# Performance work log

Hardware: AMD Instinct MI355X
Metric: run time of the kernel (lower is better)

## Reference

```python
import jax, jax.numpy as jnp
import numpy as np

HEADS = 16
HEAD_DIM = 64  # hidden_dim // heads = 1024 // 16


def setup_inputs() -> dict:
    key = jax.random.key(0)
    ks = jax.random.split(key, 7)
    B, S, D = 2, 2048, 1024
    x = jax.random.normal(ks[0], (B, S, D), dtype=jnp.float32)
    mask = jax.random.randint(ks[1], (B, 1, S, S), 0, 2, dtype=jnp.int32)
    scale = 1.0 / np.sqrt(D)
    Wq = jax.random.normal(ks[2], (D, D), dtype=jnp.float32) * scale
    Wk = jax.random.normal(ks[3], (D, D), dtype=jnp.float32) * scale
    Wv = jax.random.normal(ks[4], (D, D), dtype=jnp.float32) * scale
    Wo = jax.random.normal(ks[5], (D, D), dtype=jnp.float32) * scale
    bo = jnp.zeros((D,), dtype=jnp.float32)
    return {"x": x, "mask": mask, "Wq": Wq, "Wk": Wk, "Wv": Wv, "Wo": Wo, "bo": bo}


def _split_heads(t):
    # (B, S, D) -> (B, H, S, Hd)
    B, S, D = t.shape
    return t.reshape(B, S, HEADS, HEAD_DIM).transpose(0, 2, 1, 3)


def reference(x, mask, Wq, Wk, Wv, Wo, bo):
    B, S, D = x.shape
    # torch nn.Linear: y = x @ W.T (weights stored [out, in])
    q = _split_heads(x @ Wq.T)
    k = _split_heads(x @ Wk.T)
    v = _split_heads(x @ Wv.T)
    scores = jnp.einsum("bhqd,bhkd->bhqk", q, k) / jnp.sqrt(jnp.float32(HEAD_DIM))
    scores = jnp.where(mask == 1, jnp.float32(-1e9), scores)
    attn = jax.nn.softmax(scores, axis=-1)
    # dropout p=0.0 (eval) -> identity
    out = jnp.einsum("bhqk,bhkd->bhqd", attn, v)
    out = out.transpose(0, 2, 1, 3).reshape(B, S, D)
    return out @ Wo.T + bo
```

## Files before the change

kernel.cpp:

```cpp
#include <hip/hip_runtime.h>
#include <hip/hip_bf16.h>

typedef __attribute__((ext_vector_type(4))) float f32x4;
typedef __attribute__((ext_vector_type(8))) short bf16x8;

#define MFMA16(a, b, c) __builtin_amdgcn_mfma_f32_16x16x32_bf16(a, b, c, 0, 0, 0)

#define AS1(p) ((const __attribute__((address_space(1))) void*)(p))
#define AS3(p) ((__attribute__((address_space(3))) void*)(p))

#define SWZ(r) ((((r) & 7)) ^ ((((r) >> 3) & 1) << 2))

__device__ __forceinline__ unsigned short f2bf(float f) {
  union { float f; unsigned u; } x; x.f = f;
  unsigned r = x.u + 0x7fffu + ((x.u >> 16) & 1u);
  return (unsigned short)(r >> 16);
}

__global__ __launch_bounds__(256) void convert_all(
    const float* __restrict__ x, const float* __restrict__ wq,
    const float* __restrict__ wk, const float* __restrict__ wv,
    const float* __restrict__ wo, unsigned short* __restrict__ dst) {
  const int NX = 4194304, NW = 1048576, TOT = NX + 4 * NW;
  for (int i = blockIdx.x * 256 + threadIdx.x; i < TOT; i += gridDim.x * 256) {
    float v;
    if (i < NX) {
      v = x[i];
    } else {
      int j = i - NX; int ws = j >> 20; int o = j & (NW - 1);
      v = (ws == 0) ? wq[o] : (ws == 1) ? wk[o] : (ws == 2) ? wv[o] : wo[o];
    }
    dst[i] = f2bf(v);
  }
}

__global__ __launch_bounds__(256) void convert_mask(
    const int* __restrict__ m, unsigned char* __restrict__ o) {
  const int i = blockIdx.x * 256 + threadIdx.x;
  const int4 v = ((const int4*)m)[i];
  uchar4 r;
  r.x = (unsigned char)v.x; r.y = (unsigned char)v.y;
  r.z = (unsigned char)v.z; r.w = (unsigned char)v.w;
  ((uchar4*)o)[i] = r;
}

__device__ __forceinline__ void gemm_nt_128(
    const unsigned short* __restrict__ A, const unsigned short* __restrict__ Bw,
    int m0, int n0, unsigned short* Al, unsigned short* Bl, f32x4 acc[4][4]) {
  const int t = threadIdx.x;
  const int l = t & 63;
  const int w = t >> 6, wr = w >> 1, wc = w & 1;
  const int lc = l & 15, lg = l >> 4;

  auto stage = [&](int buf, int kt) {
    const int k0 = kt * 32;
#pragma unroll
    for (int c = 0; c < 2; ++c) {
      const int e = (t + c * 256) * 8;
      const int row = e >> 5, col = e & 31;
      __builtin_amdgcn_global_load_lds(
          AS1(A + (size_t)(m0 + row) * 1024 + k0 + col),
          AS3(Al + buf * 4096 + (w * 64 + c * 256) * 8), 16, 0, 0);
      __builtin_amdgcn_global_load_lds(
          AS1(Bw + (size_t)(n0 + row) * 1024 + k0 + col),
          AS3(Bl + buf * 4096 + (w * 64 + c * 256) * 8), 16, 0, 0);
    }
  };

  stage(0, 0);
#pragma unroll 2
  for (int kt = 0; kt < 32; ++kt) {
    __syncthreads();
    if (kt + 1 < 32) stage((kt + 1) & 1, kt + 1);
    const unsigned short* Ab = Al + (kt & 1) * 4096;
    const unsigned short* Bb = Bl + (kt & 1) * 4096;
    bf16x8 af[4], bfr[4];
#pragma unroll
    for (int i = 0; i < 4; ++i)
      af[i] = *(const bf16x8*)(Ab + (wr * 64 + i * 16 + lc) * 32 + lg * 8);
#pragma unroll
    for (int j = 0; j < 4; ++j)
      bfr[j] = *(const bf16x8*)(Bb + (wc * 64 + j * 16 + lc) * 32 + lg * 8);
#pragma unroll
    for (int i = 0; i < 4; ++i)
#pragma unroll
      for (int j = 0; j < 4; ++j)
        acc[i][j] = MFMA16(af[i], bfr[j], acc[i][j]);
  }
}

__global__ __launch_bounds__(256) void gemm_qkv(
    const unsigned short* __restrict__ xb,
    const unsigned short* __restrict__ wqb, const unsigned short* __restrict__ wkb,
    const unsigned short* __restrict__ wvb,
    unsigned short* __restrict__ q, unsigned short* __restrict__ k,
    unsigned short* __restrict__ vt) {
  __shared__ unsigned short Al[2 * 4096], Bl[2 * 4096];
  const int z = blockIdx.z;
  const unsigned short* Bw = (z == 0) ? wqb : (z == 1) ? wkb : wvb;
  const int m0 = blockIdx.x * 128, n0 = blockIdx.y * 128;
  f32x4 acc[4][4] = {};
  gemm_nt_128(xb, Bw, m0, n0, Al, Bl, acc);

  const int l = threadIdx.x & 63, w = threadIdx.x >> 6;
  const int wr = w >> 1, wc = w & 1, lc = l & 15, lg = l >> 4;

  if (z == 2) {
#pragma unroll
    for (int i = 0; i < 4; ++i)
#pragma unroll
      for (int j = 0; j < 4; ++j) {
        const int m = m0 + wr * 64 + i * 16 + lg * 4;
        const int n = n0 + wc * 64 + j * 16 + lc;
        const int b = m >> 11, s = m & 2047, hh = n >> 6, hd = n & 63;
        ushort4 pk;
        pk.x = f2bf(acc[i][j][0]); pk.y = f2bf(acc[i][j][1]);
        pk.z = f2bf(acc[i][j][2]); pk.w = f2bf(acc[i][j][3]);
        *(ushort4*)(vt + (size_t)((b << 4) + hh) * 131072 + (size_t)hd * 2048 + s) = pk;
      }
  } else {
    unsigned short* C = (z == 0) ? q : k;
#pragma unroll
    for (int i = 0; i < 4; ++i)
#pragma unroll
      for (int j = 0; j < 4; ++j)
#pragma unroll
        for (int r = 0; r < 4; ++r) {
          const int m = m0 + wr * 64 + i * 16 + lg * 4 + r;
          const int n = n0 + wc * 64 + j * 16 + lc;
          const int b = m >> 11, s = m & 2047, hh = n >> 6, hd = n & 63;
          C[(size_t)((b << 4) + hh) * 131072 + s * 64 + hd] = f2bf(acc[i][j][r]);
        }
  }
}

__global__ __launch_bounds__(256) void gemm_out(
    const unsigned short* __restrict__ ao, const unsigned short* __restrict__ wob,
    const float* __restrict__ bias, float* __restrict__ out) {
  __shared__ unsigned short Al[2 * 4096], Bl[2 * 4096];
  const int m0 = blockIdx.x * 128, n0 = blockIdx.y * 128;
  f32x4 acc[4][4] = {};
  gemm_nt_128(ao, wob, m0, n0, Al, Bl, acc);

  const int l = threadIdx.x & 63, w = threadIdx.x >> 6;
  const int wr = w >> 1, wc = w & 1, lc = l & 15, lg = l >> 4;
#pragma unroll
  for (int i = 0; i < 4; ++i)
#pragma unroll
    for (int j = 0; j < 4; ++j)
#pragma unroll
      for (int r = 0; r < 4; ++r) {
        const int m = m0 + wr * 64 + i * 16 + lg * 4 + r;
        const int n = n0 + wc * 64 + j * 16 + lc;
        out[(size_t)m * 1024 + n] = acc[i][j][r] + bias[n];
      }
}

__global__ __launch_bounds__(256, 4) void attn_fwd(
    const unsigned short* __restrict__ q, const unsigned short* __restrict__ k,
    const unsigned short* __restrict__ vt, const unsigned char* __restrict__ mb8,
    unsigned short* __restrict__ ao) {
  __shared__ unsigned short Kl[2][4096];
  __shared__ unsigned short Vl[2][4096];
  __shared__ unsigned short Pl[4][1024];
  const int orig = blockIdx.x;
  const int nid = (orig & 7) * 128 + (orig >> 3);
  const int bh = nid >> 5, b = bh >> 4;
  const int q0 = (nid & 31) * 64;
  const int t = threadIdx.x, l = t & 63, w = t >> 6;
  const int lc = l & 15, lg = l >> 4;

  const unsigned short* qp = q + ((size_t)bh * 2048 + q0 + w * 16) * 64;
  bf16x8 qa[2];
  qa[0] = *(const bf16x8*)(qp + lc * 64 + lg * 8);
  qa[1] = *(const bf16x8*)(qp + lc * 64 + 32 + lg * 8);

  bf16x8 onesf;
#pragma unroll
  for (int j = 0; j < 8; ++j) ((unsigned short*)&onesf)[j] = (lc == 0) ? 0x3F80 : 0;

  const unsigned short* kp = k + (size_t)bh * 131072;
  const unsigned short* vp = vt + (size_t)bh * 131072;
  const unsigned char* mp = mb8 + (size_t)b * 4194304 + (size_t)(q0 + w * 16 + lc) * 2048;

  f32x4 oa[4] = {};
  f32x4 lsum = {};

  auto stage = [&](int buf, int kv0) {
#pragma unroll
    for (int c = 0; c < 2; ++c) {
      const int ldc = (c * 4 + w) * 64 + l;
      const int row = ldc >> 3, ch = ldc & 7;
      const int sch = ch ^ SWZ(row);
      __builtin_amdgcn_global_load_lds(
          AS1(kp + (size_t)(kv0 + row) * 64 + sch * 8),
          AS3(&Kl[buf][(c * 4 + w) * 512]), 16, 0, 0);
      __builtin_amdgcn_global_load_lds(
          AS1(vp + (size_t)row * 2048 + kv0 + sch * 8),
          AS3(&Vl[buf][(c * 4 + w) * 512]), 16, 0, 0);
    }
  };

  stage(0, 0);
  for (int tt = 0; tt < 32; ++tt) {
    const int kv0 = tt * 64;
    __syncthreads();
    if (tt + 1 < 32) stage((tt + 1) & 1, kv0 + 64);
    const unsigned short* Kb = Kl[tt & 1];
    const unsigned short* Vb = Vl[tt & 1];

    f32x4 sa[4];
#pragma unroll
    for (int cb = 0; cb < 4; ++cb) {
      const unsigned mw = *(const unsigned*)(mp + kv0 + cb * 16 + lg * 4);
      sa[cb][0] = -240000.f * (float)(mw & 255u);
      sa[cb][1] = -240000.f * (float)((mw >> 8) & 255u);
      sa[cb][2] = -240000.f * (float)((mw >> 16) & 255u);
      sa[cb][3] = -240000.f * (float)(mw >> 24);
    }

#pragma unroll
    for (int cb = 0; cb < 4; ++cb) {
      const int row = cb * 16 + lc;
#pragma unroll
      for (int h2 = 0; h2 < 2; ++h2) {
        bf16x8 kf = *(const bf16x8*)(Kb + row * 64 + ((h2 * 4 + lg) ^ SWZ(row)) * 8);
        sa[cb] = MFMA16(kf, qa[h2], sa[cb]);
      }
    }

    unsigned short* Pw = (unsigned short*)Pl[w];
#pragma unroll
    for (int cb = 0; cb < 4; ++cb) {
      float2 ab, cd;
      ab.x = __builtin_amdgcn_exp2f(sa[cb][0] * 0.18033688f);
      ab.y = __builtin_amdgcn_exp2f(sa[cb][1] * 0.18033688f);
      cd.x = __builtin_amdgcn_exp2f(sa[cb][2] * 0.18033688f);
      cd.y = __builtin_amdgcn_exp2f(sa[cb][3] * 0.18033688f);
      __hip_bfloat162 lo = __float22bfloat162_rn(ab);
      __hip_bfloat162 hi = __float22bfloat162_rn(cd);
      uint2 pk;
      pk.x = *(unsigned*)&lo;
      pk.y = *(unsigned*)&hi;
      *(uint2*)(Pw + lc * 64 + ((cb * 2 + (lg >> 1)) ^ SWZ(lc)) * 8 + (lg & 1) * 4) = pk;
    }

#pragma unroll
    for (int kk = 0; kk < 2; ++kk) {
      bf16x8 pa = *(const bf16x8*)(Pw + lc * 64 + ((kk * 4 + lg) ^ SWZ(lc)) * 8);
      lsum = MFMA16(pa, onesf, lsum);
#pragma unroll
      for (int db = 0; db < 4; ++db) {
        const int d = db * 16 + lc;
        bf16x8 vf = *(const bf16x8*)(Vb + d * 64 + ((kk * 4 + lg) ^ SWZ(d)) * 8);
        oa[db] = MFMA16(pa, vf, oa[db]);
      }
    }
  }

  float li[4];
#pragma unroll
  for (int r = 0; r < 4; ++r) li[r] = __shfl(lsum[r], l & 48, 64);
#pragma unroll
  for (int r = 0; r < 4; ++r) {
    const float inv = 1.0f / li[r];
    const int row = q0 + w * 16 + lg * 4 + r;
    unsigned short* dst = ao + ((size_t)b * 2048 + row) * 1024 + (bh & 15) * 64;
#pragma unroll
    for (int db = 0; db < 4; ++db) dst[db * 16 + lc] = f2bf(oa[db][r] * inv);
  }
}

extern "C" void kernel_launch(void* const* d_in, const int* in_sizes, int n_in,
                              void* d_out, int out_size, void* d_ws, size_t ws_size,
                              hipStream_t stream) {
  const float* x = (const float*)d_in[0];
  const int* mask = (const int*)d_in[1];
  const float* Wq = (const float*)d_in[2];
  const float* Wk = (const float*)d_in[3];
  const float* Wv = (const float*)d_in[4];
  const float* Wo = (const float*)d_in[5];
  const float* bo = (const float*)d_in[6];

  unsigned short* ws = (unsigned short*)d_ws;
  unsigned short* xb = ws;
  unsigned short* wqb = xb + 4194304;
  unsigned short* wkb = wqb + 1048576;
  unsigned short* wvb = wkb + 1048576;
  unsigned short* wob = wvb + 1048576;
  unsigned short* qb = wob + 1048576;
  unsigned short* kb = qb + 4194304;
  unsigned short* vtb = kb + 4194304;
  unsigned short* aob = vtb + 4194304;

  unsigned char* mb8 = (unsigned char*)xb;

  convert_all<<<dim3(4096), dim3(256), 0, stream>>>(x, Wq, Wk, Wv, Wo, ws);
  gemm_qkv<<<dim3(32, 8, 3), dim3(256), 0, stream>>>(xb, wqb, wkb, wvb, qb, kb, vtb);
  convert_mask<<<dim3(8192), dim3(256), 0, stream>>>(mask, mb8);
  attn_fwd<<<dim3(1024), dim3(256), 0, stream>>>(qb, kb, vtb, mb8, aob);
  gemm_out<<<dim3(32, 8), dim3(256), 0, stream>>>(aob, wob, bo, (float*)d_out);
}
```

Measured before the change: 269.0 us.

## Vectorize conversion, shrink attention KV tile, use smaller out-proj tiles

The fp32-to-bf16 conversion kernel now has each thread convert 8 contiguous elements with float4 loads and one 16-byte store, replacing the grid-stride scalar loop. The attention kernel halves its K/V tile from 64 to 32 keys per iteration, adds a V-specific LDS swizzle, and raises the occupancy hint to 8 blocks per CU to improve latency hiding. The GEMM helper is templated so the output projection can use 64x128 tiles with twice as many blocks, which fills more CUs. The trade-off is more loop iterations and barriers in attention, and less data reuse per block in the output GEMM.

```diff
diff --git a/kernel.cpp b/kernel.cpp
--- a/kernel.cpp
+++ b/kernel.cpp
@@ -9,7 +9,8 @@
 #define AS1(p) ((const __attribute__((address_space(1))) void*)(p))
 #define AS3(p) ((__attribute__((address_space(3))) void*)(p))
 
-#define SWZ(r) ((((r) & 7)) ^ ((((r) >> 3) & 1) << 2))
+#define SWZK(r) ((((r) & 7)) ^ ((((r) >> 3) & 1) << 2))
+#define SWZV(r) ((((r) & 3)) ^ ((((r) >> 2) & 1) << 1))
 
 __device__ __forceinline__ unsigned short f2bf(float f) {
   union { float f; unsigned u; } x; x.f = f;
@@ -21,17 +22,23 @@
     const float* __restrict__ x, const float* __restrict__ wq,
     const float* __restrict__ wk, const float* __restrict__ wv,
     const float* __restrict__ wo, unsigned short* __restrict__ dst) {
-  const int NX = 4194304, NW = 1048576, TOT = NX + 4 * NW;
-  for (int i = blockIdx.x * 256 + threadIdx.x; i < TOT; i += gridDim.x * 256) {
-    float v;
-    if (i < NX) {
-      v = x[i];
-    } else {
-      int j = i - NX; int ws = j >> 20; int o = j & (NW - 1);
-      v = (ws == 0) ? wq[o] : (ws == 1) ? wk[o] : (ws == 2) ? wv[o] : wo[o];
-    }
-    dst[i] = f2bf(v);
-  }
+  const int i = blockIdx.x * 256 + threadIdx.x;
+  const long base = (long)i * 8;
+  const int NX = 4194304, NW = 1048576;
+  const float* src; long off;
+  if (base < NX) { src = x; off = base; }
+  else {
+    long j = base - NX; int ws = (int)(j >> 20); off = j & (NW - 1);
+    src = (ws == 0) ? wq : (ws == 1) ? wk : (ws == 2) ? wv : wo;
+  }
+  float4 a = *(const float4*)(src + off);
+  float4 b = *(const float4*)(src + off + 4);
+  uint4 o;
+  o.x = (unsigned)f2bf(a.x) | ((unsigned)f2bf(a.y) << 16);
+  o.y = (unsigned)f2bf(a.z) | ((unsigned)f2bf(a.w) << 16);
+  o.z = (unsigned)f2bf(b.x) | ((unsigned)f2bf(b.y) << 16);
+  o.w = (unsigned)f2bf(b.z) | ((unsigned)f2bf(b.w) << 16);
+  ((uint4*)dst)[i] = o;
 }
 
 __global__ __launch_bounds__(256) void convert_mask(
@@ -44,26 +51,32 @@
   ((uchar4*)o)[i] = r;
 }
 
-__device__ __forceinline__ void gemm_nt_128(
+template <int BM, int BN>
+__device__ __forceinline__ void gemm_nt(
     const unsigned short* __restrict__ A, const unsigned short* __restrict__ Bw,
-    int m0, int n0, unsigned short* Al, unsigned short* Bl, f32x4 acc[4][4]) {
+    int m0, int n0, unsigned short* Al, unsigned short* Bl, f32x4* acc) {
   const int t = threadIdx.x;
   const int l = t & 63;
   const int w = t >> 6, wr = w >> 1, wc = w & 1;
   const int lc = l & 15, lg = l >> 4;
+  constexpr int MI = BM / 32, NJ = BN / 32;
+  constexpr int ASZ = BM * 32, BSZ = BN * 32;
 
   auto stage = [&](int buf, int kt) {
     const int k0 = kt * 32;
 #pragma unroll
-    for (int c = 0; c < 2; ++c) {
+    for (int c = 0; c < BM / 64; ++c) {
       const int e = (t + c * 256) * 8;
-      const int row = e >> 5, col = e & 31;
       __builtin_amdgcn_global_load_lds(
-          AS1(A + (size_t)(m0 + row) * 1024 + k0 + col),
-          AS3(Al + buf * 4096 + (w * 64 + c * 256) * 8), 16, 0, 0);
+          AS1(A + (size_t)(m0 + (e >> 5)) * 1024 + k0 + (e & 31)),
+          AS3(Al + buf * ASZ + e), 16, 0, 0);
+    }
+#pragma unroll
+    for (int c = 0; c < BN / 64; ++c) {
+      const int e = (t + c * 256) * 8;
       __builtin_amdgcn_global_load_lds(
-          AS1(Bw + (size_t)(n0 + row) * 1024 + k0 + col),
-          AS3(Bl + buf * 4096 + (w * 64 + c * 256) * 8), 16, 0, 0);
+          AS1(Bw + (size_t)(n0 + (e >> 5)) * 1024 + k0 + (e & 31)),
+          AS3(Bl + buf * BSZ + e), 16, 0, 0);
     }
   };
 
@@ -72,20 +85,20 @@
   for (int kt = 0; kt < 32; ++kt) {
     __syncthreads();
     if (kt + 1 < 32) stage((kt + 1) & 1, kt + 1);
-    const unsigned short* Ab = Al + (kt & 1) * 4096;
-    const unsigned short* Bb = Bl + (kt & 1) * 4096;
-    bf16x8 af[4], bfr[4];
-#pragma unroll
-    for (int i = 0; i < 4; ++i)
-      af[i] = *(const bf16x8*)(Ab + (wr * 64 + i * 16 + lc) * 32 + lg * 8);
-#pragma unroll
-    for (int j = 0; j < 4; ++j)
-      bfr[j] = *(const bf16x8*)(Bb + (wc * 64 + j * 16 + lc) * 32 + lg * 8);
-#pragma unroll
-    for (int i = 0; i < 4; ++i)
-#pragma unroll
-      for (int j = 0; j < 4; ++j)
-        acc[i][j] = MFMA16(af[i], bfr[j], acc[i][j]);
+    const unsigned short* Ab = Al + (kt & 1) * ASZ;
+    const unsigned short* Bb = Bl + (kt & 1) * BSZ;
+    bf16x8 af[MI], bfr[NJ];
+#pragma unroll
+    for (int i = 0; i < MI; ++i)
+      af[i] = *(const bf16x8*)(Ab + (wr * (BM / 2) + i * 16 + lc) * 32 + lg * 8);
+#pragma unroll
+    for (int j = 0; j < NJ; ++j)
+      bfr[j] = *(const bf16x8*)(Bb + (wc * (BN / 2) + j * 16 + lc) * 32 + lg * 8);
+#pragma unroll
+    for (int i = 0; i < MI; ++i)
+#pragma unroll
+      for (int j = 0; j < NJ; ++j)
+        acc[i * NJ + j] = MFMA16(af[i], bfr[j], acc[i * NJ + j]);
   }
 }
 
@@ -99,8 +112,8 @@
   const int z = blockIdx.z;
   const unsigned short* Bw = (z == 0) ? wqb : (z == 1) ? wkb : wvb;
   const int m0 = blockIdx.x * 128, n0 = blockIdx.y * 128;
-  f32x4 acc[4][4] = {};
-  gemm_nt_128(xb, Bw, m0, n0, Al, Bl, acc);
+  f32x4 acc[16] = {};
+  gemm_nt<128, 128>(xb, Bw, m0, n0, Al, Bl, acc);
 
   const int l = threadIdx.x & 63, w = threadIdx.x >> 6;
   const int wr = w >> 1, wc = w & 1, lc = l & 15, lg = l >> 4;
@@ -114,8 +127,8 @@
         const int n = n0 + wc * 64 + j * 16 + lc;
         const int b = m >> 11, s = m & 2047, hh = n >> 6, hd = n & 63;
         ushort4 pk;
-        pk.x = f2bf(acc[i][j][0]); pk.y = f2bf(acc[i][j][1]);
-        pk.z = f2bf(acc[i][j][2]); pk.w = f2bf(acc[i][j][3]);
+        pk.x = f2bf(acc[i * 4 + j][0]); pk.y = f2bf(acc[i * 4 + j][1]);
+        pk.z = f2bf(acc[i * 4 + j][2]); pk.w = f2bf(acc[i * 4 + j][3]);
         *(ushort4*)(vt + (size_t)((b << 4) + hh) * 131072 + (size_t)hd * 2048 + s) = pk;
       }
   } else {
@@ -129,7 +142,7 @@
           const int m = m0 + wr * 64 + i * 16 + lg * 4 + r;
           const int n = n0 + wc * 64 + j * 16 + lc;
           const int b = m >> 11, s = m & 2047, hh = n >> 6, hd = n & 63;
-          C[(size_t)((b << 4) + hh) * 131072 + s * 64 + hd] = f2bf(acc[i][j][r]);
+          C[(size_t)((b << 4) + hh) * 131072 + s * 64 + hd] = f2bf(acc[i * 4 + j][r]);
         }
   }
 }
@@ -137,32 +150,32 @@
 __global__ __launch_bounds__(256) void gemm_out(
     const unsigned short* __restrict__ ao, const unsigned short* __restrict__ wob,
     const float* __restrict__ bias, float* __restrict__ out) {
-  __shared__ unsigned short Al[2 * 4096], Bl[2 * 4096];
-  const int m0 = blockIdx.x * 128, n0 = blockIdx.y * 128;
-  f32x4 acc[4][4] = {};
-  gemm_nt_128(ao, wob, m0, n0, Al, Bl, acc);
+  __shared__ unsigned short Al[2 * 2048], Bl[2 * 4096];
+  const int m0 = blockIdx.x * 64, n0 = blockIdx.y * 128;
+  f32x4 acc[8] = {};
+  gemm_nt<64, 128>(ao, wob, m0, n0, Al, Bl, acc);
 
   const int l = threadIdx.x & 63, w = threadIdx.x >> 6;
   const int wr = w >> 1, wc = w & 1, lc = l & 15, lg = l >> 4;
 #pragma unroll
-  for (int i = 0; i < 4; ++i)
+  for (int i = 0; i < 2; ++i)
 #pragma unroll
     for (int j = 0; j < 4; ++j)
 #pragma unroll
       for (int r = 0; r < 4; ++r) {
-        const int m = m0 + wr * 64 + i * 16 + lg * 4 + r;
+        const int m = m0 + wr * 32 + i * 16 + lg * 4 + r;
         const int n = n0 + wc * 64 + j * 16 + lc;
-        out[(size_t)m * 1024 + n] = acc[i][j][r] + bias[n];
+        out[(size_t)m * 1024 + n] = acc[i * 4 + j][r] + bias[n];
       }
 }
 
-__global__ __launch_bounds__(256, 4) void attn_fwd(
+__global__ __launch_bounds__(256, 8) void attn_fwd(
     const unsigned short* __restrict__ q, const unsigned short* __restrict__ k,
     const unsigned short* __restrict__ vt, const unsigned char* __restrict__ mb8,
     unsigned short* __restrict__ ao) {
-  __shared__ unsigned short Kl[2][4096];
-  __shared__ unsigned short Vl[2][4096];
-  __shared__ unsigned short Pl[4][1024];
+  __shared__ unsigned short Kl[2][2048];
+  __shared__ unsigned short Vl[2][2048];
+  __shared__ unsigned short Pl[4][512];
   const int orig = blockIdx.x;
   const int nid = (orig & 7) * 128 + (orig >> 3);
   const int bh = nid >> 5, b = bh >> 4;
@@ -187,31 +200,34 @@
   f32x4 lsum = {};
 
   auto stage = [&](int buf, int kv0) {
-#pragma unroll
-    for (int c = 0; c < 2; ++c) {
-      const int ldc = (c * 4 + w) * 64 + l;
+    const int ldc = w * 64 + l;
+    {
       const int row = ldc >> 3, ch = ldc & 7;
-      const int sch = ch ^ SWZ(row);
+      const int sch = ch ^ SWZK(row);
       __builtin_amdgcn_global_load_lds(
           AS1(kp + (size_t)(kv0 + row) * 64 + sch * 8),
-          AS3(&Kl[buf][(c * 4 + w) * 512]), 16, 0, 0);
+          AS3(&Kl[buf][(size_t)w * 512]), 16, 0, 0);
+    }
+    {
+      const int row = ldc >> 2, ch = ldc & 3;
+      const int sch = ch ^ SWZV(row);
       __builtin_amdgcn_global_load_lds(
           AS1(vp + (size_t)row * 2048 + kv0 + sch * 8),
-          AS3(&Vl[buf][(c * 4 + w) * 512]), 16, 0, 0);
+          AS3(&Vl[buf][(size_t)w * 512]), 16, 0, 0);
     }
   };
 
   stage(0, 0);
-  for (int tt = 0; tt < 32; ++tt) {
-    const int kv0 = tt * 64;
+  for (int tt = 0; tt < 64; ++tt) {
+    const int kv0 = tt * 32;
     __syncthreads();
-    if (tt + 1 < 32) stage((tt + 1) & 1, kv0 + 64);
+    if (tt + 1 < 64) stage((tt + 1) & 1, kv0 + 32);
     const unsigned short* Kb = Kl[tt & 1];
     const unsigned short* Vb = Vl[tt & 1];
 
-    f32x4 sa[4];
-#pragma unroll
-    for (int cb = 0; cb < 4; ++cb) {
+    f32x4 sa[2];
+#pragma unroll
+    for (int cb = 0; cb < 2; ++cb) {
       const unsigned mw = *(const unsigned*)(mp + kv0 + cb * 16 + lg * 4);
       sa[cb][0] = -240000.f * (float)(mw & 255u);
       sa[cb][1] = -240000.f * (float)((mw >> 8) & 255u);
@@ -220,18 +236,18 @@
     }
 
 #pragma unroll
-    for (int cb = 0; cb < 4; ++cb) {
+    for (int cb = 0; cb < 2; ++cb) {
       const int row = cb * 16 + lc;
 #pragma unroll
       for (int h2 = 0; h2 < 2; ++h2) {
-        bf16x8 kf = *(const bf16x8*)(Kb + row * 64 + ((h2 * 4 + lg) ^ SWZ(row)) * 8);
+        bf16x8 kf = *(const bf16x8*)(Kb + row * 64 + ((h2 * 4 + lg) ^ SWZK(row)) * 8);
         sa[cb] = MFMA16(kf, qa[h2], sa[cb]);
       }
     }
 
     unsigned short* Pw = (unsigned short*)Pl[w];
 #pragma unroll
-    for (int cb = 0; cb < 4; ++cb) {
+    for (int cb = 0; cb < 2; ++cb) {
       float2 ab, cd;
       ab.x = __builtin_amdgcn_exp2f(sa[cb][0] * 0.18033688f);
       ab.y = __builtin_amdgcn_exp2f(sa[cb][1] * 0.18033688f);
@@ -242,19 +258,16 @@
       uint2 pk;
       pk.x = *(unsigned*)&lo;
       pk.y = *(unsigned*)&hi;
-      *(uint2*)(Pw + lc * 64 + ((cb * 2 + (lg >> 1)) ^ SWZ(lc)) * 8 + (lg & 1) * 4) = pk;
-    }
-
-#pragma unroll
-    for (int kk = 0; kk < 2; ++kk) {
-      bf16x8 pa = *(const bf16x8*)(Pw + lc * 64 + ((kk * 4 + lg) ^ SWZ(lc)) * 8);
-      lsum = MFMA16(pa, onesf, lsum);
-#pragma unroll
-      for (int db = 0; db < 4; ++db) {
-        const int d = db * 16 + lc;
-        bf16x8 vf = *(const bf16x8*)(Vb + d * 64 + ((kk * 4 + lg) ^ SWZ(d)) * 8);
-        oa[db] = MFMA16(pa, vf, oa[db]);
-      }
+      *(uint2*)(Pw + lc * 32 + ((cb * 2 + (lg >> 1)) ^ SWZV(lc)) * 8 + (lg & 1) * 4) = pk;
+    }
+
+    bf16x8 pa = *(const bf16x8*)(Pw + lc * 32 + (lg ^ SWZV(lc)) * 8);
+    lsum = MFMA16(pa, onesf, lsum);
+#pragma unroll
+    for (int db = 0; db < 4; ++db) {
+      const int d = db * 16 + lc;
+      bf16x8 vf = *(const bf16x8*)(Vb + d * 32 + (lg ^ SWZV(d)) * 8);
+      oa[db] = MFMA16(pa, vf, oa[db]);
     }
   }
 
@@ -295,9 +308,9 @@
 
   unsigned char* mb8 = (unsigned char*)xb;
 
-  convert_all<<<dim3(4096), dim3(256), 0, stream>>>(x, Wq, Wk, Wv, Wo, ws);
+  convert_all<<<dim3(15360), dim3(256), 0, stream>>>(x, Wq, Wk, Wv, Wo, ws);
   gemm_qkv<<<dim3(32, 8, 3), dim3(256), 0, stream>>>(xb, wqb, wkb, wvb, qb, kb, vtb);
   convert_mask<<<dim3(8192), dim3(256), 0, stream>>>(mask, mb8);
   attn_fwd<<<dim3(1024), dim3(256), 0, stream>>>(qb, kb, vtb, mb8, aob);
-  gemm_out<<<dim3(32, 8), dim3(256), 0, stream>>>(aob, wob, bo, (float*)d_out);
-}
+  gemm_out<<<dim3(64, 8), dim3(256), 0, stream>>>(aob, wob, bo, (float*)d_out);
+}
```

Measured after the change: 292.0 us. 1.09x slower.
